# Optimization experiments

Measured on AMD Instinct MI355X. Metric: run time of the kernel, lower is better.

## Reference

```python
import jax, jax.numpy as jnp
import numpy as np


def setup_inputs() -> dict:
    key = jax.random.key(0)
    k1, k2 = jax.random.split(key)
    B, H, W = 32, 512, 512
    H_SHAPE = (3, 3)  # filter shape -> w has h0*h1 - 1 = 8 taps
    x = jax.random.normal(k1, (B, H, W, 1), dtype=jnp.float32)
    w = jax.random.uniform(k2, (1, H_SHAPE[0] * H_SHAPE[1] - 1), dtype=jnp.float32)
    return {"x": x, "w": w}


def reference(x, w):
    # x: [B, H, W, 1] float32, w: [1, h0*h1-1] float32
    B, H, W = x.shape[0], x.shape[1], x.shape[2]
    xm = x.reshape(-1, H, W)  # [B, H, W]

    # Zero-pad the filter taps to the full [H, W] grid (top-left placement).
    hm1 = jnp.pad(w, ((0, H - w.shape[0]), (0, W - w.shape[1])))

    cplx = jnp.complex64
    # Inverse filter spectrum and its three flipped/rolled (frequency-reversed) copies.
    gm1f = 1.0 / jnp.fft.fft2(hm1.astype(cplx))                 # [H, W]
    gm2f = jnp.roll(jnp.flip(gm1f, axis=0), shift=1, axis=0)
    gm3f = jnp.roll(jnp.flip(gm1f, axis=1), shift=1, axis=1)
    gm4f = jnp.roll(jnp.flip(gm3f, axis=0), shift=1, axis=0)
    gmf = (gm1f * gm2f) * (gm3f * gm4f)                         # [H, W]

    # Apply combined inverse filter in the frequency domain.
    ymf = gmf * jnp.fft.fft2(xm.astype(cplx))                   # [B, H, W]
    ym = jnp.real(jnp.fft.ifft2(ymf)).astype(jnp.float32)       # tf.cast complex->float takes real part
    return ym.reshape(-1, H, W, 1)
```

## Files before the change

kernel.cpp:

```cpp
#include <hip/hip_runtime.h>


#define WDIM 512

struct cplx { float re, im; };
__device__ __forceinline__ cplx cadd(cplx a, cplx b) { return {a.re + b.re, a.im + b.im}; }
__device__ __forceinline__ cplx csub(cplx a, cplx b) { return {a.re - b.re, a.im - b.im}; }
__device__ __forceinline__ cplx cmul(cplx a, cplx b) {
    return {a.re * b.re - a.im * b.im, a.re * b.im + a.im * b.re};
}
template <int SIGN> __device__ __forceinline__ cplx cmul_i(cplx a) {
    return (SIGN > 0) ? cplx{-a.im, a.re} : cplx{a.im, -a.re};
}
__device__ __forceinline__ cplx twmul(cplx v, float c, float s) {
    return {v.re * c - v.im * s, v.im * c + v.re * s};
}

template <int SIGN> __device__ __forceinline__ void dft8(const cplx* a, cplx* b) {
    cplx t0 = cadd(a[0], a[4]), t4 = csub(a[0], a[4]);
    cplx t1 = cadd(a[1], a[5]), t5 = csub(a[1], a[5]);
    cplx t2 = cadd(a[2], a[6]), t6 = cmul_i<SIGN>(csub(a[2], a[6]));
    cplx t3 = cadd(a[3], a[7]), t7 = cmul_i<SIGN>(csub(a[3], a[7]));
    cplx E0 = cadd(t0, t2), E2 = csub(t0, t2);
    cplx E1 = cadd(t4, t6), E3 = csub(t4, t6);
    cplx O0 = cadd(t1, t3), O2 = csub(t1, t3);
    cplx O1 = cadd(t5, t7), O3 = csub(t5, t7);
    const float C = 0.70710678118654752f;
    cplx w1 = {C, SIGN * C};
    cplx w3 = {-C, SIGN * C};
    cplx O1w = cmul(O1, w1);
    cplx O2w = cmul_i<SIGN>(O2);
    cplx O3w = cmul(O3, w3);
    b[0] = cadd(E0, O0);  b[4] = csub(E0, O0);
    b[1] = cadd(E1, O1w); b[5] = csub(E1, O1w);
    b[2] = cadd(E2, O2w); b[6] = csub(E2, O2w);
    b[3] = cadd(E3, O3w); b[7] = csub(E3, O3w);
}

__device__ __forceinline__ int phi(int q) { return q + ((q >> 6) << 1); }

__global__ __launch_bounds__(64, 4) void fft_conv_kernel(const float* __restrict__ x,
                                                         const float* __restrict__ w,
                                                         float* __restrict__ y) {
    __shared__ float2 l[528];
    const int u = threadIdx.x;
    const int pair = blockIdx.x;
    const float* x1 = x + (size_t)(2 * pair) * WDIM;
    const float* x2 = x1 + WDIM;

    cplx a[8], b[8];
#pragma unroll
    for (int j = 0; j < 8; ++j) {
        int i = u + 64 * j;
        a[j].re = x1[i];
        a[j].im = x2[i];
    }

    float c512[7], s512[7], c64[7], s64[7];
#pragma unroll
    for (int t = 1; t < 8; ++t) {
        float f = (float)(u * t) * (1.0f / 512.0f);
        s512[t - 1] = __builtin_amdgcn_sinf(f);
        c512[t - 1] = __builtin_amdgcn_cosf(f);
        float g = (float)((u & 7) * t) * (1.0f / 64.0f);
        s64[t - 1] = __builtin_amdgcn_sinf(g);
        c64[t - 1] = __builtin_amdgcn_cosf(g);
    }

    const int base = ((u >> 3) << 6) | (u & 7);

    dft8<-1>(a, b);
#pragma unroll
    for (int t = 1; t < 8; ++t) b[t] = twmul(b[t], c512[t - 1], -s512[t - 1]);
#pragma unroll
    for (int t = 0; t < 8; ++t) l[phi(u + 64 * t)] = make_float2(b[t].re, b[t].im);
    __syncthreads();

#pragma unroll
    for (int j = 0; j < 8; ++j) {
        float2 v = l[phi(base + 8 * j)];
        a[j].re = v.x; a[j].im = v.y;
    }
    dft8<-1>(a, b);
#pragma unroll
    for (int t = 1; t < 8; ++t) b[t] = twmul(b[t], c64[t - 1], -s64[t - 1]);
#pragma unroll
    for (int t = 0; t < 8; ++t) l[phi(base + 8 * t)] = make_float2(b[t].re, b[t].im);
    __syncthreads();

    float Gv[8];
    {
        const int c = ((u & 7) << 3) | (u >> 3);
        cplx m[8], Hv[8];
        m[0].re = w[0]; m[0].im = 0.0f;
#pragma unroll
        for (int j = 1; j < 8; ++j) {
            float f = (float)(c * j) * (1.0f / 512.0f);
            float sn = __builtin_amdgcn_sinf(f);
            float cs = __builtin_amdgcn_cosf(f);
            float wj = w[j];
            m[j].re = wj * cs;
            m[j].im = -wj * sn;
        }
        dft8<-1>(m, Hv);
#pragma unroll
        for (int t = 0; t < 8; ++t) {
            float m2 = Hv[t].re * Hv[t].re + Hv[t].im * Hv[t].im;
            Gv[t] = (1.0f / 512.0f) / (m2 * m2);
        }
    }

    {
        const int cb = 8 * u;
#pragma unroll
        for (int j = 0; j < 8; ++j) {
            float2 v = l[phi(cb + j)];
            a[j].re = v.x; a[j].im = v.y;
        }
        dft8<-1>(a, b);
#pragma unroll
        for (int t = 0; t < 8; ++t) { b[t].re *= Gv[t]; b[t].im *= Gv[t]; }
        dft8<+1>(b, a);
#pragma unroll
        for (int j = 0; j < 8; ++j) l[phi(cb + j)] = make_float2(a[j].re, a[j].im);
    }
    __syncthreads();

#pragma unroll
    for (int t = 0; t < 8; ++t) {
        float2 v = l[phi(base + 8 * t)];
        a[t].re = v.x; a[t].im = v.y;
    }
#pragma unroll
    for (int t = 1; t < 8; ++t) a[t] = twmul(a[t], c64[t - 1], s64[t - 1]);
    dft8<+1>(a, b);
#pragma unroll
    for (int j = 0; j < 8; ++j) l[phi(base + 8 * j)] = make_float2(b[j].re, b[j].im);
    __syncthreads();

#pragma unroll
    for (int t = 0; t < 8; ++t) {
        float2 v = l[phi(u + 64 * t)];
        a[t].re = v.x; a[t].im = v.y;
    }
#pragma unroll
    for (int t = 1; t < 8; ++t) a[t] = twmul(a[t], c512[t - 1], s512[t - 1]);
    dft8<+1>(a, b);
    float* y1 = y + (size_t)(2 * pair) * WDIM;
    float* y2 = y1 + WDIM;
#pragma unroll
    for (int j = 0; j < 8; ++j) {
        int i = u + 64 * j;
        y1[i] = b[j].re;
        y2[i] = b[j].im;
    }
}

extern "C" void kernel_launch(void* const* d_in, const int* in_sizes, int n_in,
                              void* d_out, int out_size, void* d_ws, size_t ws_size,
                              hipStream_t stream) {
    const float* x = (const float*)d_in[0];
    const float* w = (const float*)d_in[1];
    float* y = (float*)d_out;

    fft_conv_kernel<<<dim3(8192), dim3(64), 0, stream>>>(x, w, y);
}
```

Before: 87.47 us.

## Precompute twiddles and inverse filter gains in setup kernel; use packed float2 math

Adds a one-block setup kernel that writes the twiddle factors and the per-column inverse-filter gains to workspace memory, computed from w on every call. The main kernel loads these tables instead of recomputing sin/cos and the filter DFT in each of the 8192 blocks. Complex arithmetic is also rewritten with ext_vector float2 so the compiler can emit packed FP32 instructions. The tradeoff is one extra kernel launch and extra global (cached) loads per thread in exchange for fewer transcendental ops and less ALU work.

Measured after the change: 87.12 us. No clear change (-0.4%).

```diff
diff --git a/kernel.cpp b/kernel.cpp
--- a/kernel.cpp
+++ b/kernel.cpp
@@ -3,156 +3,152 @@
 
 #define WDIM 512
 
-struct cplx { float re, im; };
-__device__ __forceinline__ cplx cadd(cplx a, cplx b) { return {a.re + b.re, a.im + b.im}; }
-__device__ __forceinline__ cplx csub(cplx a, cplx b) { return {a.re - b.re, a.im - b.im}; }
-__device__ __forceinline__ cplx cmul(cplx a, cplx b) {
-    return {a.re * b.re - a.im * b.im, a.re * b.im + a.im * b.re};
+typedef float v2f __attribute__((ext_vector_type(2)));
+
+__device__ __forceinline__ v2f mkv2(float x, float y) { v2f r; r.x = x; r.y = y; return r; }
+
+template <int SIGN> __device__ __forceinline__ v2f cmul_i(v2f a) {
+    return (SIGN > 0) ? mkv2(-a.y, a.x) : mkv2(a.y, -a.x);
 }
-template <int SIGN> __device__ __forceinline__ cplx cmul_i(cplx a) {
-    return (SIGN > 0) ? cplx{-a.im, a.re} : cplx{a.im, -a.re};
-}
-__device__ __forceinline__ cplx twmul(cplx v, float c, float s) {
-    return {v.re * c - v.im * s, v.im * c + v.re * s};
+__device__ __forceinline__ v2f twmul(v2f v, float c, float s) {
+    return v * c + cmul_i<1>(v) * s;
 }
 
-template <int SIGN> __device__ __forceinline__ void dft8(const cplx* a, cplx* b) {
-    cplx t0 = cadd(a[0], a[4]), t4 = csub(a[0], a[4]);
-    cplx t1 = cadd(a[1], a[5]), t5 = csub(a[1], a[5]);
-    cplx t2 = cadd(a[2], a[6]), t6 = cmul_i<SIGN>(csub(a[2], a[6]));
-    cplx t3 = cadd(a[3], a[7]), t7 = cmul_i<SIGN>(csub(a[3], a[7]));
-    cplx E0 = cadd(t0, t2), E2 = csub(t0, t2);
-    cplx E1 = cadd(t4, t6), E3 = csub(t4, t6);
-    cplx O0 = cadd(t1, t3), O2 = csub(t1, t3);
-    cplx O1 = cadd(t5, t7), O3 = csub(t5, t7);
+template <int SIGN> __device__ __forceinline__ void dft8(const v2f* a, v2f* b) {
+    v2f t0 = a[0] + a[4], t4 = a[0] - a[4];
+    v2f t1 = a[1] + a[5], t5 = a[1] - a[5];
+    v2f t2 = a[2] + a[6], t6 = cmul_i<SIGN>(a[2] - a[6]);
+    v2f t3 = a[3] + a[7], t7 = cmul_i<SIGN>(a[3] - a[7]);
+    v2f E0 = t0 + t2, E2 = t0 - t2;
+    v2f E1 = t4 + t6, E3 = t4 - t6;
+    v2f O0 = t1 + t3, O2 = t1 - t3;
+    v2f O1 = t5 + t7, O3 = t5 - t7;
     const float C = 0.70710678118654752f;
-    cplx w1 = {C, SIGN * C};
-    cplx w3 = {-C, SIGN * C};
-    cplx O1w = cmul(O1, w1);
-    cplx O2w = cmul_i<SIGN>(O2);
-    cplx O3w = cmul(O3, w3);
-    b[0] = cadd(E0, O0);  b[4] = csub(E0, O0);
-    b[1] = cadd(E1, O1w); b[5] = csub(E1, O1w);
-    b[2] = cadd(E2, O2w); b[6] = csub(E2, O2w);
-    b[3] = cadd(E3, O3w); b[7] = csub(E3, O3w);
+    v2f O1w = twmul(O1, C, SIGN * C);
+    v2f O2w = cmul_i<SIGN>(O2);
+    v2f O3w = twmul(O3, -C, SIGN * C);
+    b[0] = E0 + O0;  b[4] = E0 - O0;
+    b[1] = E1 + O1w; b[5] = E1 - O1w;
+    b[2] = E2 + O2w; b[6] = E2 - O2w;
+    b[3] = E3 + O3w; b[7] = E3 - O3w;
 }
 
 __device__ __forceinline__ int phi(int q) { return q + ((q >> 6) << 1); }
 
+__global__ void fft_conv_setup(const float* __restrict__ w, float* __restrict__ T) {
+    const int u = threadIdx.x;
+    v2f* t512 = (v2f*)(T + WDIM);
+    v2f* t64 = t512 + 7 * 64;
+#pragma unroll
+    for (int t = 1; t < 8; ++t) {
+        float f = (float)(u * t) * (1.0f / 512.0f);
+        t512[(t - 1) * 64 + u] = mkv2(__builtin_amdgcn_cosf(f), __builtin_amdgcn_sinf(f));
+        float g = (float)((u & 7) * t) * (1.0f / 64.0f);
+        t64[(t - 1) * 64 + u] = mkv2(__builtin_amdgcn_cosf(g), __builtin_amdgcn_sinf(g));
+    }
+    const int c = ((u & 7) << 3) | (u >> 3);
+    v2f m[8], Hv[8];
+    m[0] = mkv2(w[0], 0.0f);
+#pragma unroll
+    for (int j = 1; j < 8; ++j) {
+        float f = (float)(c * j) * (1.0f / 512.0f);
+        float sn = __builtin_amdgcn_sinf(f);
+        float cs = __builtin_amdgcn_cosf(f);
+        float wj = w[j];
+        m[j] = mkv2(wj * cs, -wj * sn);
+    }
+    dft8<-1>(m, Hv);
+    float Gv[8];
+#pragma unroll
+    for (int t = 0; t < 8; ++t) {
+        float m2 = Hv[t].x * Hv[t].x + Hv[t].y * Hv[t].y;
+        Gv[t] = (1.0f / 512.0f) / (m2 * m2);
+    }
+    float4* Gp = (float4*)T;
+    Gp[2 * u] = make_float4(Gv[0], Gv[1], Gv[2], Gv[3]);
+    Gp[2 * u + 1] = make_float4(Gv[4], Gv[5], Gv[6], Gv[7]);
+}
+
 __global__ __launch_bounds__(64, 4) void fft_conv_kernel(const float* __restrict__ x,
-                                                         const float* __restrict__ w,
+                                                         const float* __restrict__ T,
                                                          float* __restrict__ y) {
-    __shared__ float2 l[528];
+    __shared__ v2f l[528];
     const int u = threadIdx.x;
     const int pair = blockIdx.x;
     const float* x1 = x + (size_t)(2 * pair) * WDIM;
     const float* x2 = x1 + WDIM;
 
-    cplx a[8], b[8];
+    v2f a[8], b[8];
 #pragma unroll
     for (int j = 0; j < 8; ++j) {
         int i = u + 64 * j;
-        a[j].re = x1[i];
-        a[j].im = x2[i];
+        a[j] = mkv2(x1[i], x2[i]);
     }
 
-    float c512[7], s512[7], c64[7], s64[7];
+    v2f tw5[7], tw6[7];
+    const v2f* t512 = (const v2f*)(T + WDIM);
+    const v2f* t64 = t512 + 7 * 64;
 #pragma unroll
-    for (int t = 1; t < 8; ++t) {
-        float f = (float)(u * t) * (1.0f / 512.0f);
-        s512[t - 1] = __builtin_amdgcn_sinf(f);
-        c512[t - 1] = __builtin_amdgcn_cosf(f);
-        float g = (float)((u & 7) * t) * (1.0f / 64.0f);
-        s64[t - 1] = __builtin_amdgcn_sinf(g);
-        c64[t - 1] = __builtin_amdgcn_cosf(g);
+    for (int t = 0; t < 7; ++t) {
+        tw5[t] = t512[t * 64 + u];
+        tw6[t] = t64[t * 64 + u];
     }
+    const float4* Gp = (const float4*)T;
+    float4 g0 = Gp[2 * u];
+    float4 g1 = Gp[2 * u + 1];
 
     const int base = ((u >> 3) << 6) | (u & 7);
 
     dft8<-1>(a, b);
 #pragma unroll
-    for (int t = 1; t < 8; ++t) b[t] = twmul(b[t], c512[t - 1], -s512[t - 1]);
+    for (int t = 1; t < 8; ++t) b[t] = twmul(b[t], tw5[t - 1].x, -tw5[t - 1].y);
 #pragma unroll
-    for (int t = 0; t < 8; ++t) l[phi(u + 64 * t)] = make_float2(b[t].re, b[t].im);
+    for (int t = 0; t < 8; ++t) l[phi(u + 64 * t)] = b[t];
     __syncthreads();
 
 #pragma unroll
-    for (int j = 0; j < 8; ++j) {
-        float2 v = l[phi(base + 8 * j)];
-        a[j].re = v.x; a[j].im = v.y;
-    }
+    for (int j = 0; j < 8; ++j) a[j] = l[phi(base + 8 * j)];
     dft8<-1>(a, b);
 #pragma unroll
-    for (int t = 1; t < 8; ++t) b[t] = twmul(b[t], c64[t - 1], -s64[t - 1]);
+    for (int t = 1; t < 8; ++t) b[t] = twmul(b[t], tw6[t - 1].x, -tw6[t - 1].y);
 #pragma unroll
-    for (int t = 0; t < 8; ++t) l[phi(base + 8 * t)] = make_float2(b[t].re, b[t].im);
+    for (int t = 0; t < 8; ++t) l[phi(base + 8 * t)] = b[t];
     __syncthreads();
-
-    float Gv[8];
-    {
-        const int c = ((u & 7) << 3) | (u >> 3);
-        cplx m[8], Hv[8];
-        m[0].re = w[0]; m[0].im = 0.0f;
-#pragma unroll
-        for (int j = 1; j < 8; ++j) {
-            float f = (float)(c * j) * (1.0f / 512.0f);
-            float sn = __builtin_amdgcn_sinf(f);
-            float cs = __builtin_amdgcn_cosf(f);
-            float wj = w[j];
-            m[j].re = wj * cs;
-            m[j].im = -wj * sn;
-        }
-        dft8<-1>(m, Hv);
-#pragma unroll
-        for (int t = 0; t < 8; ++t) {
-            float m2 = Hv[t].re * Hv[t].re + Hv[t].im * Hv[t].im;
-            Gv[t] = (1.0f / 512.0f) / (m2 * m2);
-        }
-    }
 
     {
         const int cb = 8 * u;
 #pragma unroll
-        for (int j = 0; j < 8; ++j) {
-            float2 v = l[phi(cb + j)];
-            a[j].re = v.x; a[j].im = v.y;
-        }
+        for (int j = 0; j < 8; ++j) a[j] = l[phi(cb + j)];
         dft8<-1>(a, b);
+        b[0] *= g0.x; b[1] *= g0.y; b[2] *= g0.z; b[3] *= g0.w;
+        b[4] *= g1.x; b[5] *= g1.y; b[6] *= g1.z; b[7] *= g1.w;
+        dft8<1>(b, a);
 #pragma unroll
-        for (int t = 0; t < 8; ++t) { b[t].re *= Gv[t]; b[t].im *= Gv[t]; }
-        dft8<+1>(b, a);
-#pragma unroll
-        for (int j = 0; j < 8; ++j) l[phi(cb + j)] = make_float2(a[j].re, a[j].im);
+        for (int j = 0; j < 8; ++j) l[phi(cb + j)] = a[j];
     }
     __syncthreads();
 
 #pragma unroll
-    for (int t = 0; t < 8; ++t) {
-        float2 v = l[phi(base + 8 * t)];
-        a[t].re = v.x; a[t].im = v.y;
-    }
+    for (int t = 0; t < 8; ++t) a[t] = l[phi(base + 8 * t)];
 #pragma unroll
-    for (int t = 1; t < 8; ++t) a[t] = twmul(a[t], c64[t - 1], s64[t - 1]);
-    dft8<+1>(a, b);
+    for (int t = 1; t < 8; ++t) a[t] = twmul(a[t], tw6[t - 1].x, tw6[t - 1].y);
+    dft8<1>(a, b);
 #pragma unroll
-    for (int j = 0; j < 8; ++j) l[phi(base + 8 * j)] = make_float2(b[j].re, b[j].im);
+    for (int j = 0; j < 8; ++j) l[phi(base + 8 * j)] = b[j];
     __syncthreads();
 
 #pragma unroll
-    for (int t = 0; t < 8; ++t) {
-        float2 v = l[phi(u + 64 * t)];
-        a[t].re = v.x; a[t].im = v.y;
-    }
+    for (int t = 0; t < 8; ++t) a[t] = l[phi(u + 64 * t)];
 #pragma unroll
-    for (int t = 1; t < 8; ++t) a[t] = twmul(a[t], c512[t - 1], s512[t - 1]);
-    dft8<+1>(a, b);
+    for (int t = 1; t < 8; ++t) a[t] = twmul(a[t], tw5[t - 1].x, tw5[t - 1].y);
+    dft8<1>(a, b);
     float* y1 = y + (size_t)(2 * pair) * WDIM;
     float* y2 = y1 + WDIM;
 #pragma unroll
     for (int j = 0; j < 8; ++j) {
         int i = u + 64 * j;
-        y1[i] = b[j].re;
-        y2[i] = b[j].im;
+        y1[i] = b[j].x;
+        y2[i] = b[j].y;
     }
 }
 
@@ -162,6 +158,8 @@
     const float* x = (const float*)d_in[0];
     const float* w = (const float*)d_in[1];
     float* y = (float*)d_out;
+    float* T = (float*)d_ws;
 
-    fft_conv_kernel<<<dim3(8192), dim3(64), 0, stream>>>(x, w, y);
+    fft_conv_setup<<<dim3(1), dim3(64), 0, stream>>>(w, T);
+    fft_conv_kernel<<<dim3(8192), dim3(64), 0, stream>>>(x, T, y);
 }
```
